# Kernel optimization log

Hardware: AMD Instinct MI355X
Metric: run time of the kernel (lower is better)

The kernel has to match this reference:

```python
import jax, jax.numpy as jnp
import numpy as np

B, H, W_SP, C = 256, 14, 14, 768
NUM_CLASSES = 701


def setup_inputs() -> dict:
    key = jax.random.key(0)
    k1, k2, k3 = jax.random.split(key, 3)
    x1 = jax.random.normal(k1, (B, H, W_SP, C), dtype=jnp.float32)
    x2 = jax.random.normal(k2, (B, H, W_SP, C), dtype=jnp.float32)
    W = jax.random.normal(k3, (C, NUM_CLASSES), dtype=jnp.float32) * 0.02
    b = jnp.zeros((NUM_CLASSES,), dtype=jnp.float32)
    return {"x1": x1, "x2": x2, "W": W, "b": b}


def _sgm(feats):
    """Vectorized SGM: per-sample sort by normalized token energy, gap-based
    split index, masked means for background/foreground. feats: [B, N, C]."""
    n = feats.shape[1]
    M = feats.sum(axis=-1)                                  # [B, N] token energies
    mn = M.min(axis=-1, keepdims=True)
    mx = M.max(axis=-1, keepdims=True)
    Mn = (M - mn) / (mx - mn)                               # normalized to [0,1]
    order = jnp.argsort(Mn, axis=-1)                        # ascending
    sorted_tens = jnp.take_along_axis(feats, order[:, :, None], axis=1)  # [B,N,C]
    sorted_M = jnp.take_along_axis(Mn, order, axis=-1)      # [B, N]
    # diff[j] = M[j+1]-M[j], forced to 0 where M[j]==0 (as in original)
    diff = jnp.where(sorted_M[:, :-1] == 0.0, 0.0,
                     sorted_M[:, 1:] - sorted_M[:, :-1])    # [B, N-1]
    k = jnp.argmax(diff, axis=-1)                           # [B] split index
    idx = jnp.arange(n)[None, :]                            # [1, N]
    fg_mask = (idx < k[:, None]).astype(feats.dtype)        # rows [:k] -> foreground
    bg_mask = 1.0 - fg_mask                                 # rows [k:] -> background
    fg_cnt = jnp.maximum(k.astype(feats.dtype), 1.0)[:, None]
    bg_cnt = jnp.maximum((n - k).astype(feats.dtype), 1.0)[:, None]
    foregr = jnp.einsum('bnc,bn->bc', sorted_tens, fg_mask) / fg_cnt
    backgr = jnp.einsum('bnc,bn->bc', sorted_tens, bg_mask) / bg_cnt
    return backgr, foregr


def reference(x1, x2, W, b):
    # flatten spatial dims into a token axis: [B, H*W, C]
    f1 = x1.reshape(x1.shape[0], -1, x1.shape[-1])
    f2 = x2.reshape(x2.shape[0], -1, x2.shape[-1])
    x1_bg, x1_fg = _sgm(f1)
    x2_bg, x2_fg = _sgm(f2)
    classif = lambda v: v @ W + b
    return (classif(x1_bg), classif(x1_fg), classif(x2_bg), classif(x2_fg))
```

## Files before the change

### kernel.cpp

```cpp
#include <hip/hip_runtime.h>
#include <hip/hip_bf16.h>

#define NTOK 196
#define CDIM 768
#define BSAMP 256
#define NCLS 701
#define NCLSP 704

typedef __attribute__((ext_vector_type(8))) short bf16x8;
typedef __attribute__((ext_vector_type(4))) float f32x4;

__device__ __forceinline__ void add4(float4& a, const float4& b) {
  a.x += b.x; a.y += b.y; a.z += b.z; a.w += b.w;
}

__global__ __launch_bounds__(512) void sgm_kernel(const float* __restrict__ x1,
                                                  const float* __restrict__ x2,
                                                  __hip_bfloat16* __restrict__ Vb) {
  const int task = blockIdx.x;
  const int s  = task & 255;
  const int br = task >> 8;
  const float* __restrict__ feats = (br ? x2 : x1) + (size_t)s * (NTOK * CDIM);

  const int tid  = threadIdx.x;
  const int lane = tid & 63;
  const int wv   = tid >> 6;

  __shared__ float Msh[NTOK];
  __shared__ float Mn[NTOK];
  __shared__ float sortedv[NTOK];
  __shared__ int   rnk[NTOK];
  __shared__ int   list[NTOK];
  __shared__ float redmin[8], redmax[8];
  __shared__ int   kSh;
  __shared__ int   cntSh;
  __shared__ float partS[8][CDIM];
  __shared__ float partT[8][CDIM];

  float4 acc[3];
  #pragma unroll
  for (int g = 0; g < 3; g++) acc[g] = make_float4(0.f, 0.f, 0.f, 0.f);

  const float* lanebase = feats + lane * 4;

  for (int ib = 0; ib < 6; ib++) {
    const int t0 = wv + ib * 32;
    const float* p = lanebase + (size_t)t0 * CDIM;
    float4 r[4][3];
    #pragma unroll
    for (int j = 0; j < 4; j++)
      #pragma unroll
      for (int g = 0; g < 3; g++)
        r[j][g] = *(const float4*)(p + j * (8 * CDIM) + g * 256);

    float e[4];
    #pragma unroll
    for (int j = 0; j < 4; j++) {
      #pragma unroll
      for (int g = 0; g < 3; g++) add4(acc[g], r[j][g]);
      e[j] = ((r[j][0].x + r[j][0].y) + (r[j][0].z + r[j][0].w))
           + ((r[j][1].x + r[j][1].y) + (r[j][1].z + r[j][1].w))
           + ((r[j][2].x + r[j][2].y) + (r[j][2].z + r[j][2].w));
    }
    #pragma unroll
    for (int off = 32; off; off >>= 1) {
      #pragma unroll
      for (int j = 0; j < 4; j++) e[j] += __shfl_xor(e[j], off);
    }
    if (lane == 0) {
      #pragma unroll
      for (int j = 0; j < 4; j++) Msh[t0 + j * 8] = e[j];
    }
  }
  if (wv < 4) {
    const int t = 192 + wv;
    const float* p = lanebase + (size_t)t * CDIM;
    float4 r0 = *(const float4*)(p);
    float4 r1 = *(const float4*)(p + 256);
    float4 r2 = *(const float4*)(p + 512);
    add4(acc[0], r0); add4(acc[1], r1); add4(acc[2], r2);
    float e = ((r0.x + r0.y) + (r0.z + r0.w))
            + ((r1.x + r1.y) + (r1.z + r1.w))
            + ((r2.x + r2.y) + (r2.z + r2.w));
    #pragma unroll
    for (int off = 32; off; off >>= 1) e += __shfl_xor(e, off);
    if (lane == 0) Msh[t] = e;
  }
  if (tid == 0) cntSh = 0;
  __syncthreads();

  float vmn = (tid < NTOK) ? Msh[tid] :  1e30f;
  float vmx = (tid < NTOK) ? Msh[tid] : -1e30f;
  #pragma unroll
  for (int off = 32; off; off >>= 1) {
    vmn = fminf(vmn, __shfl_xor(vmn, off));
    vmx = fmaxf(vmx, __shfl_xor(vmx, off));
  }
  if (lane == 0) { redmin[wv] = vmn; redmax[wv] = vmx; }
  __syncthreads();
  float mn = redmin[0], mx = redmax[0];
  #pragma unroll
  for (int i = 1; i < 8; i++) { mn = fminf(mn, redmin[i]); mx = fmaxf(mx, redmax[i]); }
  const float rng = mx - mn;
  if (tid < NTOK) Mn[tid] = (Msh[tid] - mn) / rng;
  __syncthreads();

  if (tid < NTOK) {
    const float mv = Mn[tid];
    int r = 0;
    for (int u = 0; u < NTOK; u++) {
      const float o = Mn[u];
      r += (o < mv) || (o == mv && u < tid);
    }
    sortedv[r] = mv;
    rnk[tid] = r;
  }
  __syncthreads();

  if (tid < 64) {
    float bd = -1.0f; int bj = NTOK;
    for (int j = lane; j < NTOK - 1; j += 64) {
      const float sj = sortedv[j];
      const float d = (sj == 0.0f) ? 0.0f : (sortedv[j + 1] - sj);
      if (d > bd || (d == bd && j < bj)) { bd = d; bj = j; }
    }
    #pragma unroll
    for (int off = 32; off; off >>= 1) {
      const float od = __shfl_xor(bd, off);
      const int   oj = __shfl_xor(bj, off);
      if (od > bd || (od == bd && oj < bj)) { bd = od; bj = oj; }
    }
    if (lane == 0) kSh = bj;
  }
  __syncthreads();

  const int k = kSh;
  const bool takeFg = (k <= NTOK / 2);

  if (tid < NTOK) {
    const int r = rnk[tid];
    const bool inSet = takeFg ? (r < k) : (r >= k);
    if (inSet) { int p = atomicAdd(&cntSh, 1); list[p] = tid; }
  }
  __syncthreads();
  const int m = cntSh;

  float4 tacc[3];
  #pragma unroll
  for (int g = 0; g < 3; g++) tacc[g] = make_float4(0.f, 0.f, 0.f, 0.f);

  for (int i0 = wv * 4; i0 < m; i0 += 32) {
    const int nb = m - i0;
    float4 r[4][3];
    #pragma unroll
    for (int j = 0; j < 4; j++) {
      if (j < nb) {
        const int t = list[i0 + j];
        const float* p = lanebase + (size_t)t * CDIM;
        #pragma unroll
        for (int g = 0; g < 3; g++) r[j][g] = *(const float4*)(p + g * 256);
      }
    }
    #pragma unroll
    for (int j = 0; j < 4; j++) {
      if (j < nb) {
        #pragma unroll
        for (int g = 0; g < 3; g++) add4(tacc[g], r[j][g]);
      }
    }
  }

  const int base = lane * 4;
  #pragma unroll
  for (int g = 0; g < 3; g++) {
    *(float4*)&partS[wv][base + g * 256] = acc[g];
    *(float4*)&partT[wv][base + g * 256] = tacc[g];
  }
  __syncthreads();

  const float fgc = (float)(k > 1 ? k : 1);
  const float bgc = (float)((NTOK - k) > 1 ? (NTOK - k) : 1);
  const size_t rowFg = (size_t)(2 * br + 1) * BSAMP + s;
  const size_t rowBg = (size_t)(2 * br    ) * BSAMP + s;
  for (int c = tid; c < CDIM; c += 512) {
    float S = 0.0f, T = 0.0f;
    #pragma unroll
    for (int w = 0; w < 8; w++) { S += partS[w][c]; T += partT[w][c]; }
    float fg, bg;
    if (takeFg) { fg = T;     bg = S - T; }
    else        { bg = T;     fg = S - T; }
    Vb[rowFg * CDIM + c] = __float2bfloat16(fg / fgc);
    Vb[rowBg * CDIM + c] = __float2bfloat16(bg / bgc);
  }
}

__global__ __launch_bounds__(256) void wt_kernel(const float* __restrict__ W,
                                                 __hip_bfloat16* __restrict__ WT) {
  __shared__ float tile[32][33];
  const int c0 = blockIdx.x * 32;
  const int k0 = blockIdx.y * 32;
  const int tx = threadIdx.x & 31;
  const int ty = threadIdx.x >> 5;
  #pragma unroll
  for (int i = 0; i < 4; i++) {
    const int kr = ty + i * 8;
    const int c = c0 + tx;
    tile[kr][tx] = (c < NCLS) ? W[(size_t)(k0 + kr) * NCLS + c] : 0.0f;
  }
  __syncthreads();
  #pragma unroll
  for (int i = 0; i < 4; i++) {
    const int cr = ty + i * 8;
    const int cls = c0 + cr;
    WT[(size_t)cls * CDIM + k0 + tx] = __float2bfloat16(tile[tx][cr]);
  }
}

__global__ __launch_bounds__(256) void mfma_gemm(const __hip_bfloat16* __restrict__ Vb,
                                                 const __hip_bfloat16* __restrict__ WT,
                                                 const float* __restrict__ bias,
                                                 float* __restrict__ out) {
  const int w = blockIdx.x * 4 + (threadIdx.x >> 6);
  const int lane = threadIdx.x & 63;
  const int tr = w / (NCLSP / 16);
  const int tc = w % (NCLSP / 16);
  const int m0 = tr * 16;
  const int n0 = tc * 16;
  const int ko = (lane >> 4) * 8;

  const short* aptr = (const short*)Vb + (size_t)(m0 + (lane & 15)) * CDIM + ko;
  const short* bptr = (const short*)WT + (size_t)(n0 + (lane & 15)) * CDIM + ko;

  f32x4 acc = {0.f, 0.f, 0.f, 0.f};
  #pragma unroll
  for (int k0 = 0; k0 < CDIM; k0 += 32) {
    const bf16x8 af = *(const bf16x8*)(aptr + k0);
    const bf16x8 bf = *(const bf16x8*)(bptr + k0);
    acc = __builtin_amdgcn_mfma_f32_16x16x32_bf16(af, bf, acc, 0, 0, 0);
  }

  const int crow = m0 + (lane >> 4) * 4;
  const int ccol = n0 + (lane & 15);
  if (ccol < NCLS) {
    const float bv = bias[ccol];
    #pragma unroll
    for (int r = 0; r < 4; r++)
      out[(size_t)(crow + r) * NCLS + ccol] = acc[r] + bv;
  }
}

extern "C" void kernel_launch(void* const* d_in, const int* in_sizes, int n_in,
                              void* d_out, int out_size, void* d_ws, size_t ws_size,
                              hipStream_t stream) {
  const float* x1 = (const float*)d_in[0];
  const float* x2 = (const float*)d_in[1];
  const float* W  = (const float*)d_in[2];
  const float* b  = (const float*)d_in[3];
  float* out = (float*)d_out;

  __hip_bfloat16* Vb = (__hip_bfloat16*)d_ws;
  __hip_bfloat16* WT = (__hip_bfloat16*)((char*)d_ws + 1024 * CDIM * 2);

  sgm_kernel<<<512, 512, 0, stream>>>(x1, x2, Vb);
  wt_kernel<<<dim3(22, 24), 256, 0, stream>>>(W, WT);
  mfma_gemm<<<704, 256, 0, stream>>>(Vb, WT, b, out);
}
```

Measured before the change: 348.9 us.

## Stream token tiles into LDS via double-buffered global_load_lds in SGM kernel

Replaces the direct register loads of token rows in both the energy/sum pass and the selected-subset pass with asynchronous global-to-LDS loads (16 bytes per lane) into a two-stage buffer of 8 tokens each. Each wave then reads one token row from LDS per tile. Explicit vmcnt waits and barriers overlap the next tile's fetch with the current tile's reduction. The LDS buffers are reused as the partial-sum arrays, and waves with no real row issue dummy loads so the wait counts stay fixed. This adds two barriers per tile and an LDS round trip, and the previous code already kept several 16-byte loads in flight per thread.

```diff
diff --git a/kernel.cpp b/kernel.cpp
--- a/kernel.cpp
+++ b/kernel.cpp
@@ -6,12 +6,20 @@
 #define BSAMP 256
 #define NCLS 701
 #define NCLSP 704
+#define TILE 8
+#define NTA 25
 
 typedef __attribute__((ext_vector_type(8))) short bf16x8;
 typedef __attribute__((ext_vector_type(4))) float f32x4;
 
 __device__ __forceinline__ void add4(float4& a, const float4& b) {
   a.x += b.x; a.y += b.y; a.z += b.z; a.w += b.w;
+}
+
+__device__ __forceinline__ void g2l16(const float* g, float* l) {
+  __builtin_amdgcn_global_load_lds(
+      (const __attribute__((address_space(1))) void*)g,
+      (__attribute__((address_space(3))) void*)l, 16, 0, 0);
 }
 
 __global__ __launch_bounds__(512) void sgm_kernel(const float* __restrict__ x1,
@@ -26,6 +34,8 @@
   const int lane = tid & 63;
   const int wv   = tid >> 6;
 
+  __shared__ float buf[2][TILE][CDIM];
+  __shared__ float dummy[256];
   __shared__ float Msh[NTOK];
   __shared__ float Mn[NTOK];
   __shared__ float sortedv[NTOK];
@@ -34,58 +44,55 @@
   __shared__ float redmin[8], redmax[8];
   __shared__ int   kSh;
   __shared__ int   cntSh;
-  __shared__ float partS[8][CDIM];
-  __shared__ float partT[8][CDIM];
 
   float4 acc[3];
   #pragma unroll
   for (int g = 0; g < 3; g++) acc[g] = make_float4(0.f, 0.f, 0.f, 0.f);
 
-  const float* lanebase = feats + lane * 4;
-
-  for (int ib = 0; ib < 6; ib++) {
-    const int t0 = wv + ib * 32;
-    const float* p = lanebase + (size_t)t0 * CDIM;
-    float4 r[4][3];
-    #pragma unroll
-    for (int j = 0; j < 4; j++)
+  auto issueA = [&](int t) {
+    const int nreal3 = (t < NTA - 1) ? 24 : 12;
+    float (*bq)[CDIM] = buf[t & 1];
+    #pragma unroll
+    for (int ii = 0; ii < 3; ii++) {
+      const int i = wv + ii * 8;
+      if (i < nreal3) {
+        const int j = i / 3, g = i % 3;
+        g2l16(feats + (size_t)(t * TILE + j) * CDIM + g * 256 + lane * 4,
+              &bq[j][g * 256]);
+      } else {
+        g2l16(feats + lane * 4, dummy);
+      }
+    }
+  };
+
+  issueA(0);
+  for (int t = 0; t < NTA; t++) {
+    if (t + 1 < NTA) {
+      issueA(t + 1);
+      asm volatile("s_waitcnt vmcnt(3)" ::: "memory");
+    } else {
+      asm volatile("s_waitcnt vmcnt(0)" ::: "memory");
+    }
+    __builtin_amdgcn_s_barrier();
+
+    const int tok = t * TILE + wv;
+    if (tok < NTOK) {
+      const float* row = buf[t & 1][wv];
+      const float4 r0 = *(const float4*)(row + lane * 4);
+      const float4 r1 = *(const float4*)(row + lane * 4 + 256);
+      const float4 r2 = *(const float4*)(row + lane * 4 + 512);
+      add4(acc[0], r0); add4(acc[1], r1); add4(acc[2], r2);
+      float e = ((r0.x + r0.y) + (r0.z + r0.w))
+              + ((r1.x + r1.y) + (r1.z + r1.w))
+              + ((r2.x + r2.y) + (r2.z + r2.w));
       #pragma unroll
-      for (int g = 0; g < 3; g++)
-        r[j][g] = *(const float4*)(p + j * (8 * CDIM) + g * 256);
-
-    float e[4];
-    #pragma unroll
-    for (int j = 0; j < 4; j++) {
-      #pragma unroll
-      for (int g = 0; g < 3; g++) add4(acc[g], r[j][g]);
-      e[j] = ((r[j][0].x + r[j][0].y) + (r[j][0].z + r[j][0].w))
-           + ((r[j][1].x + r[j][1].y) + (r[j][1].z + r[j][1].w))
-           + ((r[j][2].x + r[j][2].y) + (r[j][2].z + r[j][2].w));
-    }
-    #pragma unroll
-    for (int off = 32; off; off >>= 1) {
-      #pragma unroll
-      for (int j = 0; j < 4; j++) e[j] += __shfl_xor(e[j], off);
-    }
-    if (lane == 0) {
-      #pragma unroll
-      for (int j = 0; j < 4; j++) Msh[t0 + j * 8] = e[j];
-    }
-  }
-  if (wv < 4) {
-    const int t = 192 + wv;
-    const float* p = lanebase + (size_t)t * CDIM;
-    float4 r0 = *(const float4*)(p);
-    float4 r1 = *(const float4*)(p + 256);
-    float4 r2 = *(const float4*)(p + 512);
-    add4(acc[0], r0); add4(acc[1], r1); add4(acc[2], r2);
-    float e = ((r0.x + r0.y) + (r0.z + r0.w))
-            + ((r1.x + r1.y) + (r1.z + r1.w))
-            + ((r2.x + r2.y) + (r2.z + r2.w));
-    #pragma unroll
-    for (int off = 32; off; off >>= 1) e += __shfl_xor(e, off);
-    if (lane == 0) Msh[t] = e;
-  }
+      for (int off = 32; off; off >>= 1) e += __shfl_xor(e, off);
+      if (lane == 0) Msh[tok] = e;
+    }
+    asm volatile("s_waitcnt lgkmcnt(0)" ::: "memory");
+    __builtin_amdgcn_s_barrier();
+  }
+
   if (tid == 0) cntSh = 0;
   __syncthreads();
 
@@ -149,27 +156,50 @@
   #pragma unroll
   for (int g = 0; g < 3; g++) tacc[g] = make_float4(0.f, 0.f, 0.f, 0.f);
 
-  for (int i0 = wv * 4; i0 < m; i0 += 32) {
-    const int nb = m - i0;
-    float4 r[4][3];
-    #pragma unroll
-    for (int j = 0; j < 4; j++) {
-      if (j < nb) {
-        const int t = list[i0 + j];
-        const float* p = lanebase + (size_t)t * CDIM;
-        #pragma unroll
-        for (int g = 0; g < 3; g++) r[j][g] = *(const float4*)(p + g * 256);
+  const int nct = (m + TILE - 1) / TILE;
+
+  auto issueC = [&](int t) {
+    const int rem = m - t * TILE;
+    const int nreal3 = (rem >= TILE ? TILE : rem) * 3;
+    float (*bq)[CDIM] = buf[t & 1];
+    #pragma unroll
+    for (int ii = 0; ii < 3; ii++) {
+      const int i = wv + ii * 8;
+      if (i < nreal3) {
+        const int j = i / 3, g = i % 3;
+        const int tok = list[t * TILE + j];
+        g2l16(feats + (size_t)tok * CDIM + g * 256 + lane * 4,
+              &bq[j][g * 256]);
+      } else {
+        g2l16(feats + lane * 4, dummy);
       }
     }
-    #pragma unroll
-    for (int j = 0; j < 4; j++) {
-      if (j < nb) {
-        #pragma unroll
-        for (int g = 0; g < 3; g++) add4(tacc[g], r[j][g]);
-      }
-    }
-  }
-
+  };
+
+  if (nct > 0) issueC(0);
+  for (int t = 0; t < nct; t++) {
+    if (t + 1 < nct) {
+      issueC(t + 1);
+      asm volatile("s_waitcnt vmcnt(3)" ::: "memory");
+    } else {
+      asm volatile("s_waitcnt vmcnt(0)" ::: "memory");
+    }
+    __builtin_amdgcn_s_barrier();
+
+    const int li = t * TILE + wv;
+    if (li < m) {
+      const float* row = buf[t & 1][wv];
+      const float4 r0 = *(const float4*)(row + lane * 4);
+      const float4 r1 = *(const float4*)(row + lane * 4 + 256);
+      const float4 r2 = *(const float4*)(row + lane * 4 + 512);
+      add4(tacc[0], r0); add4(tacc[1], r1); add4(tacc[2], r2);
+    }
+    asm volatile("s_waitcnt lgkmcnt(0)" ::: "memory");
+    __builtin_amdgcn_s_barrier();
+  }
+
+  float (*partS)[CDIM] = (float (*)[CDIM])buf[0];
+  float (*partT)[CDIM] = (float (*)[CDIM])buf[1];
   const int base = lane * 4;
   #pragma unroll
   for (int g = 0; g < 3; g++) {
```

Result: no change. 349.4 us (+0.1%).
